# Kernel optimization log

Measured on AMD Instinct MI355X. Metric: run time of the kernel, lower is better.

Reference implementation:

```python
import jax, jax.numpy as jnp
import numpy as np

N = 100000
E = 3200000
IN_DIM = 64
HID = 64
G = 4096
BN_EPS = 1e-5


def setup_inputs() -> dict:
    key = jax.random.key(0)
    ks = jax.random.split(key, 20)
    def lin(k, fi, fo):
        bound = 1.0 / np.sqrt(fi)
        kw, kb = jax.random.split(k)
        W = jax.random.uniform(kw, (fi, fo), jnp.float32, -bound, bound)
        b = jax.random.uniform(kb, (fo,), jnp.float32, -bound, bound)
        return W, b
    x = jax.random.normal(ks[0], (N, IN_DIM), jnp.float32)
    edge_index = jax.random.randint(ks[1], (2, E), 0, N, jnp.int64)
    batch = jnp.sort(jax.random.randint(ks[2], (N,), 0, G, jnp.int64))
    proj_W, proj_b = lin(ks[3], IN_DIM, HID)
    conv1_W, conv1_b = lin(ks[4], HID, HID)
    conv2_W, conv2_b = lin(ks[5], HID, HID)
    conv3_W, conv3_b = lin(ks[6], HID, HID)
    head_W1, head_b1 = lin(ks[7], HID, HID // 2)
    head_W2, head_b2 = lin(ks[8], HID // 2, 1)
    ones = jnp.ones((HID,), jnp.float32)
    zeros = jnp.zeros((HID,), jnp.float32)
    return dict(
        x=x, edge_index=edge_index, batch=batch,
        proj_W=proj_W, proj_b=proj_b,
        conv1_W=conv1_W, conv1_b=conv1_b,
        conv2_W=conv2_W, conv2_b=conv2_b,
        conv3_W=conv3_W, conv3_b=conv3_b,
        bn1_g=ones, bn1_b=zeros, bn2_g=ones, bn2_b=zeros,
        bn3_g=ones, bn3_b=zeros,
        head_W1=head_W1, head_b1=head_b1,
        head_W2=head_W2, head_b2=head_b2,
    )


def _gcn_conv(x, W, b, src, dst, dinv):
    # GCNConv with self-loops and symmetric normalization (PyG semantics).
    xl = x @ W                                   # [N, H]
    norm = dinv[src] * dinv[dst]                 # [E]
    msg = xl[src] * norm[:, None]                # [E, H]  (memory-bound gather)
    agg = jax.ops.segment_sum(msg, dst, num_segments=x.shape[0])
    agg = agg + (dinv * dinv)[:, None] * xl      # self-loop contribution
    return agg + b


def _bn(h, g, b):
    mu = jnp.mean(h, axis=0)
    var = jnp.var(h, axis=0)
    return (h - mu) * jax.lax.rsqrt(var + BN_EPS) * g + b


def reference(x, edge_index, batch,
              proj_W, proj_b,
              conv1_W, conv1_b, conv2_W, conv2_b, conv3_W, conv3_b,
              bn1_g, bn1_b, bn2_g, bn2_b, bn3_g, bn3_b,
              head_W1, head_b1, head_W2, head_b2):
    src, dst = edge_index[0], edge_index[1]
    n = x.shape[0]
    # degree including self loop
    deg = jax.ops.segment_sum(jnp.ones_like(dst, jnp.float32), dst, num_segments=n) + 1.0
    dinv = jax.lax.rsqrt(deg)

    x0 = jax.nn.relu(x @ proj_W + proj_b)
    h = jax.nn.relu(_bn(_gcn_conv(x0, conv1_W, conv1_b, src, dst, dinv), bn1_g, bn1_b))
    h = jax.nn.relu(_bn(_gcn_conv(h, conv2_W, conv2_b, src, dst, dinv), bn2_g, bn2_b))
    h = h + x0
    h = jax.nn.relu(_bn(_gcn_conv(h, conv3_W, conv3_b, src, dst, dinv), bn3_g, bn3_b))

    # global mean pool over graphs
    sums = jax.ops.segment_sum(h, batch, num_segments=G)
    cnts = jax.ops.segment_sum(jnp.ones((n,), jnp.float32), batch, num_segments=G)
    pooled = sums / jnp.maximum(cnts, 1.0)[:, None]

    out = jax.nn.relu(pooled @ head_W1 + head_b1) @ head_W2 + head_b2
    return out.squeeze(-1)
```

## Files before the change

kernel.cpp:

```cpp
#include <hip/hip_runtime.h>
#include <hip/hip_fp16.h>

#define NNODES 100000
#define NEDGES 3200000
#define NGRAPH 4096
#define NSLOT 80
#define SBCNT 196
#define SBCAP 17504
#define P1CHUNK 4096
#define P1CAP 56
#define P1GRID 782
#define AGG_GRID 1563
#define BN_EPS 1e-5f
#define INV_N (1.0f / 100000.0f)

__global__ void k_zero_i(int* __restrict__ p, int n) {
  int i = blockIdx.x * blockDim.x + threadIdx.x;
  int st = gridDim.x * blockDim.x;
  for (; i < n; i += st) p[i] = 0;
}
__global__ void k_zero_f(float* __restrict__ p, int n) {
  int i = blockIdx.x * blockDim.x + threadIdx.x;
  int st = gridDim.x * blockDim.x;
  for (; i < n; i += st) p[i] = 0.0f;
}

__global__ void k_part1(const int* __restrict__ src, const int* __restrict__ dst,
                        int* __restrict__ sbcur, int* __restrict__ sbbuf, int e) {
  __shared__ int cnt[SBCNT];
  __shared__ int base[SBCNT];
  __shared__ int bins[SBCNT * P1CAP];
  int t = threadIdx.x;
  int start = blockIdx.x * P1CHUNK;
  int end = min(start + P1CHUNK, e);
  for (int i = t; i < SBCNT; i += 256) cnt[i] = 0;
  __syncthreads();
  for (int i = start + t; i < end; i += 256) {
    int s = src[i], d = dst[i];
    int sb = d >> 9;
    int en = (s << 9) | (d & 511);
    int pos = atomicAdd(&cnt[sb], 1);
    if (pos < P1CAP) {
      bins[sb * P1CAP + pos] = en;
    } else {
      int gp = atomicAdd(&sbcur[sb], 1);
      if (gp < SBCAP) sbbuf[(size_t)sb * SBCAP + gp] = en;
    }
  }
  __syncthreads();
  if (t < SBCNT) {
    int c = min(cnt[t], P1CAP);
    base[t] = (c > 0) ? atomicAdd(&sbcur[t], c) : 0;
  }
  __syncthreads();
  int lane = t & 63, wid = t >> 6;
  for (int b = wid; b < SBCNT; b += 4) {
    int c = min(cnt[b], P1CAP);
    if (lane < c) {
      int gp = base[b] + lane;
      if (gp < SBCAP) sbbuf[(size_t)b * SBCAP + gp] = bins[b * P1CAP + lane];
    }
  }
}

__global__ void k_part2(const int* __restrict__ sbcur, const int* __restrict__ sbbuf,
                        int* __restrict__ ncur, int* __restrict__ slots) {
  int sb = blockIdx.x >> 1;
  int half = blockIdx.x & 1;
  int cnt = min(sbcur[sb], SBCAP);
  const int* __restrict__ pb = sbbuf + (size_t)sb * SBCAP;
  int i0 = half * 256 + threadIdx.x;
  for (int i = i0; i < cnt; i += 4 * 512) {
    int i1 = i + 512, i2 = i + 1024, i3 = i + 1536;
    int e0 = pb[i];
    int e1 = (i1 < cnt) ? pb[i1] : 0;
    int e2 = (i2 < cnt) ? pb[i2] : 0;
    int e3 = (i3 < cnt) ? pb[i3] : 0;
    int d0 = (sb << 9) | (e0 & 511);
    int d1 = (sb << 9) | (e1 & 511);
    int d2 = (sb << 9) | (e2 & 511);
    int d3 = (sb << 9) | (e3 & 511);
    int p0 = atomicAdd(&ncur[d0], 1);
    int p1 = (i1 < cnt) ? atomicAdd(&ncur[d1], 1) : NSLOT;
    int p2 = (i2 < cnt) ? atomicAdd(&ncur[d2], 1) : NSLOT;
    int p3 = (i3 < cnt) ? atomicAdd(&ncur[d3], 1) : NSLOT;
    if (p0 < NSLOT) slots[(size_t)d0 * NSLOT + p0] = e0 >> 9;
    if (p1 < NSLOT) slots[(size_t)d1 * NSLOT + p1] = e1 >> 9;
    if (p2 < NSLOT) slots[(size_t)d2 * NSLOT + p2] = e2 >> 9;
    if (p3 < NSLOT) slots[(size_t)d3 * NSLOT + p3] = e3 >> 9;
  }
}

__global__ void k_dinv(const int* __restrict__ cursor, float* __restrict__ dinv, int n) {
  int i = blockIdx.x * blockDim.x + threadIdx.x;
  if (i < n) dinv[i] = rsqrtf((float)cursor[i] + 1.0f);
}

template <int PRO, bool EPI_DINV, bool EPI_BR>
__global__ void k_gemm64(const float* __restrict__ A, const float* __restrict__ W,
                         const float* __restrict__ bias, const float* __restrict__ stats,
                         const float* __restrict__ g, const float* __restrict__ bb,
                         const float* __restrict__ res, const float* __restrict__ dinv,
                         float* __restrict__ C, __half* __restrict__ Ch, int n) {
  __shared__ float Ws[64 * 64];
  __shared__ float As[64 * 64];
  __shared__ float scs[64], shs[64], bs[64];
  int t = threadIdx.x;
  {
    const float4* W4 = (const float4*)W;
    float4* Ws4 = (float4*)Ws;
    for (int i = t; i < 1024; i += 256) Ws4[i] = W4[i];
  }
  if (t < 64) {
    if (EPI_BR) bs[t] = bias[t];
    if (PRO >= 1) {
      float mu = stats[t] * INV_N;
      float var = stats[64 + t] * INV_N - mu * mu;
      float sc = g[t] * rsqrtf(var + BN_EPS);
      scs[t] = sc;
      shs[t] = bb[t] - mu * sc;
    }
  }
  int row0 = blockIdx.x * 64;
  int rows = min(64, n - row0);
  __syncthreads();
  {
    const float4* A4 = (const float4*)(A + (size_t)row0 * 64);
    const float4* R4 = (PRO == 2) ? (const float4*)(res + (size_t)row0 * 64) : nullptr;
    float4* As4 = (float4*)As;
    for (int i = t; i < rows * 16; i += 256) {
      float4 v = A4[i];
      if (PRO >= 1) {
        int c0 = (i & 15) * 4;
        v.x = fmaxf(fmaf(v.x, scs[c0], shs[c0]), 0.0f);
        v.y = fmaxf(fmaf(v.y, scs[c0 + 1], shs[c0 + 1]), 0.0f);
        v.z = fmaxf(fmaf(v.z, scs[c0 + 2], shs[c0 + 2]), 0.0f);
        v.w = fmaxf(fmaf(v.w, scs[c0 + 3], shs[c0 + 3]), 0.0f);
        if (PRO == 2) {
          float4 r4 = R4[i];
          v.x += r4.x; v.y += r4.y; v.z += r4.z; v.w += r4.w;
        }
      }
      As4[i] = v;
    }
  }
  __syncthreads();
  int c = t & 63;
  int w = t >> 6;
  float acc[16];
#pragma unroll
  for (int j = 0; j < 16; ++j) acc[j] = 0.0f;
#pragma unroll 4
  for (int k = 0; k < 64; ++k) {
    float wv = Ws[(k << 6) + c];
#pragma unroll
    for (int j = 0; j < 16; ++j) {
      acc[j] = fmaf(As[((w + 4 * j) << 6) + k], wv, acc[j]);
    }
  }
#pragma unroll
  for (int j = 0; j < 16; ++j) {
    int r = w + 4 * j;
    if (r < rows) {
      float o = acc[j];
      if (EPI_BR) o = fmaxf(o + bs[c], 0.0f);
      if (EPI_DINV) {
        o *= dinv[row0 + r];
        Ch[(size_t)(row0 + r) * 64 + c] = __float2half(o);
      } else {
        C[(size_t)(row0 + r) * 64 + c] = o;
      }
    }
  }
}

__global__ void k_agg(const int* __restrict__ deg, const int* __restrict__ slots,
                      const __half* __restrict__ y, const float* __restrict__ dinv,
                      float* __restrict__ ag, float* __restrict__ pstats) {
  int t = threadIdx.x;
  int lane = t & 63, wid = t >> 6;
  int wave = blockIdx.x * 4 + wid;
  int nw = gridDim.x * 4;
  float s = 0.0f, q = 0.0f;
  for (int node0 = wave; node0 < NNODES; node0 += nw) {
    int node = __builtin_amdgcn_readfirstlane(node0);
    int m = deg[node];
    if (m > NSLOT) m = NSLOT;
    const int* __restrict__ sp = slots + (size_t)node * NSLOT;
    float a0 = __half2float(y[(size_t)node * 64 + lane]);
    float a1 = 0.0f, a2 = 0.0f, a3 = 0.0f;
    float a4 = 0.0f, a5 = 0.0f, a6 = 0.0f, a7 = 0.0f;
    int k = 0;
    for (; k + 16 <= m; k += 16) {
      int s0 = sp[k + 0],  s1 = sp[k + 1],  s2 = sp[k + 2],  s3 = sp[k + 3];
      int s4 = sp[k + 4],  s5 = sp[k + 5],  s6 = sp[k + 6],  s7 = sp[k + 7];
      int s8 = sp[k + 8],  s9 = sp[k + 9],  sa = sp[k + 10], sb = sp[k + 11];
      int sc = sp[k + 12], sd = sp[k + 13], se = sp[k + 14], sf = sp[k + 15];
      __half v0 = y[(size_t)s0 * 64 + lane];
      __half v1 = y[(size_t)s1 * 64 + lane];
      __half v2 = y[(size_t)s2 * 64 + lane];
      __half v3 = y[(size_t)s3 * 64 + lane];
      __half v4 = y[(size_t)s4 * 64 + lane];
      __half v5 = y[(size_t)s5 * 64 + lane];
      __half v6 = y[(size_t)s6 * 64 + lane];
      __half v7 = y[(size_t)s7 * 64 + lane];
      __half v8 = y[(size_t)s8 * 64 + lane];
      __half v9 = y[(size_t)s9 * 64 + lane];
      __half va = y[(size_t)sa * 64 + lane];
      __half vb = y[(size_t)sb * 64 + lane];
      __half vc = y[(size_t)sc * 64 + lane];
      __half vd = y[(size_t)sd * 64 + lane];
      __half ve = y[(size_t)se * 64 + lane];
      __half vf = y[(size_t)sf * 64 + lane];
      a0 += __half2float(v0); a1 += __half2float(v1);
      a2 += __half2float(v2); a3 += __half2float(v3);
      a4 += __half2float(v4); a5 += __half2float(v5);
      a6 += __half2float(v6); a7 += __half2float(v7);
      a0 += __half2float(v8); a1 += __half2float(v9);
      a2 += __half2float(va); a3 += __half2float(vb);
      a4 += __half2float(vc); a5 += __half2float(vd);
      a6 += __half2float(ve); a7 += __half2float(vf);
    }
    for (; k + 4 <= m; k += 4) {
      int s0 = sp[k + 0], s1 = sp[k + 1], s2 = sp[k + 2], s3 = sp[k + 3];
      __half v0 = y[(size_t)s0 * 64 + lane];
      __half v1 = y[(size_t)s1 * 64 + lane];
      __half v2 = y[(size_t)s2 * 64 + lane];
      __half v3 = y[(size_t)s3 * 64 + lane];
      a0 += __half2float(v0); a1 += __half2float(v1);
      a2 += __half2float(v2); a3 += __half2float(v3);
    }
    for (; k < m; ++k) a0 += __half2float(y[(size_t)sp[k] * 64 + lane]);
    float o = dinv[node] * (((a0 + a1) + (a2 + a3)) + ((a4 + a5) + (a6 + a7)));
    ag[(size_t)node0 * 64 + lane] = o;
    s += o;
    q = fmaf(o, o, q);
  }
  __shared__ float ls[256], lq[256];
  ls[t] = s;
  lq[t] = q;
  __syncthreads();
  if (t < 64) {
    pstats[blockIdx.x * 128 + t] = ls[t] + ls[64 + t] + ls[128 + t] + ls[192 + t];
    pstats[blockIdx.x * 128 + 64 + t] = lq[t] + lq[64 + t] + lq[128 + t] + lq[192 + t];
  }
}

__global__ void k_stats_reduce(const float* __restrict__ pstats, float* __restrict__ stats) {
  __shared__ float red[256];
  int c = blockIdx.x;
  int t = threadIdx.x;
  float s = 0.0f;
  for (int i = t; i < AGG_GRID; i += 256) s += pstats[i * 128 + c];
  red[t] = s;
  __syncthreads();
  for (int o = 128; o >= 1; o >>= 1) {
    if (t < o) red[t] += red[t + o];
    __syncthreads();
  }
  if (t == 0) stats[c] = red[0];
}

__global__ void k_pool(const float* __restrict__ ag, const float* __restrict__ stats,
                       const float* __restrict__ g, const float* __restrict__ bb,
                       const int* __restrict__ batch, float* __restrict__ psum,
                       float* __restrict__ pcnt) {
  int t = threadIdx.x, lane = t & 63;
  int wave = blockIdx.x * 4 + (t >> 6);
  int c0 = wave * 32;
  if (c0 >= NNODES) return;
  float mu = stats[lane] * INV_N;
  float var = stats[64 + lane] * INV_N - mu * mu;
  float sc = g[lane] * rsqrtf(var + BN_EPS);
  float sh = bb[lane] - mu * sc;
  int gprev = -1;
  float av = 0.0f, cv = 0.0f;
  int end = min(c0 + 32, NNODES);
  for (int node = c0; node < end; ++node) {
    int gi = batch[node];
    if (gi != gprev) {
      if (gprev >= 0) {
        atomicAdd(&psum[gprev * 64 + lane], av);
        if (lane == 0) atomicAdd(&pcnt[gprev], cv);
      }
      gprev = gi;
      av = 0.0f;
      cv = 0.0f;
    }
    av += fmaxf(fmaf(ag[(size_t)node * 64 + lane], sc, sh), 0.0f);
    cv += 1.0f;
  }
  if (gprev >= 0) {
    atomicAdd(&psum[gprev * 64 + lane], av);
    if (lane == 0) atomicAdd(&pcnt[gprev], cv);
  }
}

__global__ void k_head(const float* __restrict__ psum, const float* __restrict__ pcnt,
                       const float* __restrict__ W1, const float* __restrict__ b1,
                       const float* __restrict__ W2, const float* __restrict__ b2,
                       float* __restrict__ out) {
  int gidx = blockIdx.x;
  int t = threadIdx.x;
  __shared__ float pooled[64];
  __shared__ float hid[32];
  float cnt = fmaxf(pcnt[gidx], 1.0f);
  pooled[t] = psum[gidx * 64 + t] / cnt;
  __syncthreads();
  if (t < 32) {
    float a = b1[t];
#pragma unroll
    for (int k = 0; k < 64; ++k) a = fmaf(pooled[k], W1[k * 32 + t], a);
    hid[t] = fmaxf(a, 0.0f);
  }
  __syncthreads();
  if (t == 0) {
    float o = b2[0];
#pragma unroll
    for (int j = 0; j < 32; ++j) o = fmaf(hid[j], W2[j], o);
    out[gidx] = o;
  }
}

extern "C" void kernel_launch(void* const* d_in, const int* in_sizes, int n_in,
                              void* d_out, int out_size, void* d_ws, size_t ws_size,
                              hipStream_t stream) {
  const float* x       = (const float*)d_in[0];
  const int*   eidx    = (const int*)d_in[1];
  const int*   batch   = (const int*)d_in[2];
  const float* proj_W  = (const float*)d_in[3];
  const float* proj_b  = (const float*)d_in[4];
  const float* conv1_W = (const float*)d_in[5];
  const float* conv2_W = (const float*)d_in[7];
  const float* conv3_W = (const float*)d_in[9];
  const float* bn1_g   = (const float*)d_in[11];
  const float* bn1_b   = (const float*)d_in[12];
  const float* bn2_g   = (const float*)d_in[13];
  const float* bn2_b   = (const float*)d_in[14];
  const float* bn3_g   = (const float*)d_in[15];
  const float* bn3_b   = (const float*)d_in[16];
  const float* head_W1 = (const float*)d_in[17];
  const float* head_b1 = (const float*)d_in[18];
  const float* head_W2 = (const float*)d_in[19];
  const float* head_b2 = (const float*)d_in[20];
  float* out = (float*)d_out;

  const int N = NNODES, E = NEDGES, G = NGRAPH;
  const int* src = eidx;
  const int* dst = eidx + E;

  char* p = (char*)d_ws;
  auto align256 = [](size_t v) { return (v + 255) & ~(size_t)255; };
  int* sbcur = (int*)p;      p += align256((size_t)SBCNT * 4);
  int* ncur = (int*)p;       p += align256((size_t)N * 4);
  int* slots = (int*)p;      p += align256((size_t)N * NSLOT * 4);
  float* dinv = (float*)p;   p += align256((size_t)N * 4);
  float* x0 = (float*)p;     p += align256((size_t)N * 64 * 4);
  __half* y16 = (__half*)p;  p += align256((size_t)N * 64 * 2);
  float* ag = (float*)p;     p += align256((size_t)N * 64 * 4);
  float* pstats = (float*)p; p += align256((size_t)AGG_GRID * 128 * 4);
  float* stats1 = (float*)p; p += align256(128 * 4);
  float* stats2 = (float*)p; p += align256(128 * 4);
  float* stats3 = (float*)p; p += align256(128 * 4);
  float* psum = (float*)p;   p += align256((size_t)G * 64 * 4);
  float* pcnt = (float*)p;   p += align256((size_t)G * 4);
  int* sbbuf = (int*)x0;

  const int TB = 256;
  int gemm_grid = (N + 63) / 64;

  k_zero_i<<<1, SBCNT, 0, stream>>>(sbcur, SBCNT);
  k_zero_i<<<98, TB, 0, stream>>>(ncur, N);
  k_part1<<<P1GRID, TB, 0, stream>>>(src, dst, sbcur, sbbuf, E);
  k_part2<<<SBCNT * 2, TB, 0, stream>>>(sbcur, sbbuf, ncur, slots);
  k_dinv<<<(N + TB - 1) / TB, TB, 0, stream>>>(ncur, dinv, N);

  k_zero_f<<<(G * 64 + G + TB - 1) / TB, TB, 0, stream>>>(psum, G * 64 + G);

  k_gemm64<0, false, true><<<gemm_grid, TB, 0, stream>>>(
      x, proj_W, proj_b, nullptr, nullptr, nullptr, nullptr, nullptr, x0, nullptr, N);

  k_gemm64<0, true, false><<<gemm_grid, TB, 0, stream>>>(
      x0, conv1_W, nullptr, nullptr, nullptr, nullptr, nullptr, dinv, nullptr, y16, N);
  k_agg<<<AGG_GRID, TB, 0, stream>>>(ncur, slots, y16, dinv, ag, pstats);
  k_stats_reduce<<<128, TB, 0, stream>>>(pstats, stats1);

  k_gemm64<1, true, false><<<gemm_grid, TB, 0, stream>>>(
      ag, conv2_W, nullptr, stats1, bn1_g, bn1_b, nullptr, dinv, nullptr, y16, N);
  k_agg<<<AGG_GRID, TB, 0, stream>>>(ncur, slots, y16, dinv, ag, pstats);
  k_stats_reduce<<<128, TB, 0, stream>>>(pstats, stats2);

  k_gemm64<2, true, false><<<gemm_grid, TB, 0, stream>>>(
      ag, conv3_W, nullptr, stats2, bn2_g, bn2_b, x0, dinv, nullptr, y16, N);
  k_agg<<<AGG_GRID, TB, 0, stream>>>(ncur, slots, y16, dinv, ag, pstats);
  k_stats_reduce<<<128, TB, 0, stream>>>(pstats, stats3);

  k_pool<<<(N + 127) / 128, TB, 0, stream>>>(ag, stats3, bn3_g, bn3_b, batch, psum, pcnt);
  k_head<<<G, 64, 0, stream>>>(psum, pcnt, head_W1, head_b1, head_W2, head_b2, out);
}
```

Before: 484.5 us.

## Build compact CSR adjacency with per-superbin shared-memory counting sort

```diff
diff --git a/kernel.cpp b/kernel.cpp
--- a/kernel.cpp
+++ b/kernel.cpp
@@ -4,7 +4,6 @@
 #define NNODES 100000
 #define NEDGES 3200000
 #define NGRAPH 4096
-#define NSLOT 80
 #define SBCNT 196
 #define SBCAP 17504
 #define P1CHUNK 4096
@@ -64,36 +63,49 @@
 }
 
 __global__ void k_part2(const int* __restrict__ sbcur, const int* __restrict__ sbbuf,
-                        int* __restrict__ ncur, int* __restrict__ slots) {
-  int sb = blockIdx.x >> 1;
-  int half = blockIdx.x & 1;
-  int cnt = min(sbcur[sb], SBCAP);
+                        int* __restrict__ slots, int* __restrict__ deg,
+                        int* __restrict__ rowstart) {
+  __shared__ int cnt[512];
+  __shared__ int pfx[512];
+  __shared__ int cur[512];
+  int sb = blockIdx.x;
+  int t = threadIdx.x;
+  int n = min(sbcur[sb], SBCAP);
   const int* __restrict__ pb = sbbuf + (size_t)sb * SBCAP;
-  int i0 = half * 256 + threadIdx.x;
-  for (int i = i0; i < cnt; i += 4 * 512) {
-    int i1 = i + 512, i2 = i + 1024, i3 = i + 1536;
-    int e0 = pb[i];
-    int e1 = (i1 < cnt) ? pb[i1] : 0;
-    int e2 = (i2 < cnt) ? pb[i2] : 0;
-    int e3 = (i3 < cnt) ? pb[i3] : 0;
-    int d0 = (sb << 9) | (e0 & 511);
-    int d1 = (sb << 9) | (e1 & 511);
-    int d2 = (sb << 9) | (e2 & 511);
-    int d3 = (sb << 9) | (e3 & 511);
-    int p0 = atomicAdd(&ncur[d0], 1);
-    int p1 = (i1 < cnt) ? atomicAdd(&ncur[d1], 1) : NSLOT;
-    int p2 = (i2 < cnt) ? atomicAdd(&ncur[d2], 1) : NSLOT;
-    int p3 = (i3 < cnt) ? atomicAdd(&ncur[d3], 1) : NSLOT;
-    if (p0 < NSLOT) slots[(size_t)d0 * NSLOT + p0] = e0 >> 9;
-    if (p1 < NSLOT) slots[(size_t)d1 * NSLOT + p1] = e1 >> 9;
-    if (p2 < NSLOT) slots[(size_t)d2 * NSLOT + p2] = e2 >> 9;
-    if (p3 < NSLOT) slots[(size_t)d3 * NSLOT + p3] = e3 >> 9;
-  }
-}
-
-__global__ void k_dinv(const int* __restrict__ cursor, float* __restrict__ dinv, int n) {
+  cnt[t] = 0;
+  __syncthreads();
+  for (int i = t; i < n; i += 512) atomicAdd(&cnt[pb[i] & 511], 1);
+  __syncthreads();
+  int myc = cnt[t];
+  pfx[t] = myc;
+  __syncthreads();
+  for (int o = 1; o < 512; o <<= 1) {
+    int x = (t >= o) ? pfx[t - o] : 0;
+    __syncthreads();
+    pfx[t] += x;
+    __syncthreads();
+  }
+  int excl = pfx[t] - myc;
+  int node = sb * 512 + t;
+  if (node < NNODES) {
+    deg[node] = myc;
+    rowstart[node] = sb * SBCAP + excl;
+  }
+  cur[t] = 0;
+  __syncthreads();
+  pfx[t] = excl;
+  __syncthreads();
+  for (int i = t; i < n; i += 512) {
+    int e = pb[i];
+    int dl = e & 511;
+    int pos = atomicAdd(&cur[dl], 1);
+    slots[(size_t)sb * SBCAP + pfx[dl] + pos] = e >> 9;
+  }
+}
+
+__global__ void k_dinv(const int* __restrict__ deg, float* __restrict__ dinv, int n) {
   int i = blockIdx.x * blockDim.x + threadIdx.x;
-  if (i < n) dinv[i] = rsqrtf((float)cursor[i] + 1.0f);
+  if (i < n) dinv[i] = rsqrtf((float)deg[i] + 1.0f);
 }
 
 template <int PRO, bool EPI_DINV, bool EPI_BR>
@@ -174,9 +186,10 @@
   }
 }
 
-__global__ void k_agg(const int* __restrict__ deg, const int* __restrict__ slots,
-                      const __half* __restrict__ y, const float* __restrict__ dinv,
-                      float* __restrict__ ag, float* __restrict__ pstats) {
+__global__ void k_agg(const int* __restrict__ deg, const int* __restrict__ rowstart,
+                      const int* __restrict__ slots, const __half* __restrict__ y,
+                      const float* __restrict__ dinv, float* __restrict__ ag,
+                      float* __restrict__ pstats) {
   int t = threadIdx.x;
   int lane = t & 63, wid = t >> 6;
   int wave = blockIdx.x * 4 + wid;
@@ -185,8 +198,7 @@
   for (int node0 = wave; node0 < NNODES; node0 += nw) {
     int node = __builtin_amdgcn_readfirstlane(node0);
     int m = deg[node];
-    if (m > NSLOT) m = NSLOT;
-    const int* __restrict__ sp = slots + (size_t)node * NSLOT;
+    const int* __restrict__ sp = slots + rowstart[node];
     float a0 = __half2float(y[(size_t)node * 64 + lane]);
     float a1 = 0.0f, a2 = 0.0f, a3 = 0.0f;
     float a4 = 0.0f, a5 = 0.0f, a6 = 0.0f, a7 = 0.0f;
@@ -352,8 +364,9 @@
   char* p = (char*)d_ws;
   auto align256 = [](size_t v) { return (v + 255) & ~(size_t)255; };
   int* sbcur = (int*)p;      p += align256((size_t)SBCNT * 4);
-  int* ncur = (int*)p;       p += align256((size_t)N * 4);
-  int* slots = (int*)p;      p += align256((size_t)N * NSLOT * 4);
+  int* deg = (int*)p;        p += align256((size_t)N * 4);
+  int* rowstart = (int*)p;   p += align256((size_t)N * 4);
+  int* slots = (int*)p;      p += align256((size_t)SBCNT * SBCAP * 4);
   float* dinv = (float*)p;   p += align256((size_t)N * 4);
   float* x0 = (float*)p;     p += align256((size_t)N * 64 * 4);
   __half* y16 = (__half*)p;  p += align256((size_t)N * 64 * 2);
@@ -370,10 +383,9 @@
   int gemm_grid = (N + 63) / 64;
 
   k_zero_i<<<1, SBCNT, 0, stream>>>(sbcur, SBCNT);
-  k_zero_i<<<98, TB, 0, stream>>>(ncur, N);
   k_part1<<<P1GRID, TB, 0, stream>>>(src, dst, sbcur, sbbuf, E);
-  k_part2<<<SBCNT * 2, TB, 0, stream>>>(sbcur, sbbuf, ncur, slots);
-  k_dinv<<<(N + TB - 1) / TB, TB, 0, stream>>>(ncur, dinv, N);
+  k_part2<<<SBCNT, 512, 0, stream>>>(sbcur, sbbuf, slots, deg, rowstart);
+  k_dinv<<<(N + TB - 1) / TB, TB, 0, stream>>>(deg, dinv, N);
 
   k_zero_f<<<(G * 64 + G + TB - 1) / TB, TB, 0, stream>>>(psum, G * 64 + G);
 
@@ -382,17 +394,17 @@
 
   k_gemm64<0, true, false><<<gemm_grid, TB, 0, stream>>>(
       x0, conv1_W, nullptr, nullptr, nullptr, nullptr, nullptr, dinv, nullptr, y16, N);
-  k_agg<<<AGG_GRID, TB, 0, stream>>>(ncur, slots, y16, dinv, ag, pstats);
+  k_agg<<<AGG_GRID, TB, 0, stream>>>(deg, rowstart, slots, y16, dinv, ag, pstats);
   k_stats_reduce<<<128, TB, 0, stream>>>(pstats, stats1);
 
   k_gemm64<1, true, false><<<gemm_grid, TB, 0, stream>>>(
       ag, conv2_W, nullptr, stats1, bn1_g, bn1_b, nullptr, dinv, nullptr, y16, N);
-  k_agg<<<AGG_GRID, TB, 0, stream>>>(ncur, slots, y16, dinv, ag, pstats);
+  k_agg<<<AGG_GRID, TB, 0, stream>>>(deg, rowstart, slots, y16, dinv, ag, pstats);
   k_stats_reduce<<<128, TB, 0, stream>>>(pstats, stats2);
 
   k_gemm64<2, true, false><<<gemm_grid, TB, 0, stream>>>(
       ag, conv3_W, nullptr, stats2, bn2_g, bn2_b, x0, dinv, nullptr, y16, N);
-  k_agg<<<AGG_GRID, TB, 0, stream>>>(ncur, slots, y16, dinv, ag, pstats);
+  k_agg<<<AGG_GRID, TB, 0, stream>>>(deg, rowstart, slots, y16, dinv, ag, pstats);
   k_stats_reduce<<<128, TB, 0, stream>>>(pstats, stats3);
 
   k_pool<<<(N + 127) / 128, TB, 0, stream>>>(ag, stats3, bn3_g, bn3_b, batch, psum, pcnt);
```

New measurement: 422.3 us. -12.8%, faster.
